# Kernel tuning notes

Measured on AMD Instinct MI355X. Metric: run time of the kernel, lower is better.

Reference implementation:

```python
import jax, jax.numpy as jnp
import numpy as np

B, N = 64, 4096          # trees per batch, leaves per complete binary tree
V, S = 21, 50            # amino-acid vocab, grammar-symbol vocab
E, H = 64, 128           # embed_dim, hidden_dim


def setup_inputs() -> dict:
    key = jax.random.key(0)
    ks = jax.random.split(key, 16)

    def lin_w(k, din, dout):
        return (jax.random.normal(k, (dout, din), jnp.float32) / np.sqrt(din)).astype(jnp.float32)

    tokens = jax.random.randint(ks[0], (B, N), 0, V, dtype=jnp.int32)
    symbols = jax.random.randint(ks[1], (B, N - 1), 0, S, dtype=jnp.int32)

    emb = jax.random.normal(ks[2], (V, E), jnp.float32) * 0.02
    emb = emb.at[0].set(0.0)  # padding_idx=0
    sym_emb = jax.random.normal(ks[3], (S, E), jnp.float32) * 0.02

    return {
        "tokens": tokens, "symbols": symbols,
        "emb": emb, "sym_emb": sym_emb,
        "Wp": lin_w(ks[4], E, H), "bp": jnp.zeros((H,), jnp.float32),
        "Wi": lin_w(ks[5], H, H), "bi": jnp.zeros((H,), jnp.float32),
        "Ui": lin_w(ks[6], H, H),
        "Wf": lin_w(ks[7], H, H), "bf": jnp.zeros((H,), jnp.float32),
        "Uf": lin_w(ks[8], H, H),
        "Wo": lin_w(ks[9], H, H), "bo": jnp.zeros((H,), jnp.float32),
        "Uo": lin_w(ks[10], H, H),
        "Wu": lin_w(ks[11], H, H), "bu": jnp.zeros((H,), jnp.float32),
        "Uu": lin_w(ks[12], H, H),
        "Wout": lin_w(ks[13], H, H), "bout": jnp.zeros((H,), jnp.float32),
    }


def _encode(tokens, symbols, emb, sym_emb, Wp, bp, Wi, bi, Ui, Wf, bf, Uf,
            Wo, bo, Uo, Wu, bu, Uu, Wout, bout):
    emb = emb.at[0].set(0.0)  # padding row contributes nothing (and gets no grad)

    # Leaf nodes: amino-acid embedding -> input_proj, no children.
    x = emb[tokens] @ Wp.T + bp                      # [B, N, H]
    i = jax.nn.sigmoid(x @ Wi.T + bi)
    o = jax.nn.sigmoid(x @ Wo.T + bo)
    u = jnp.tanh(x @ Wu.T + bu)
    c = i * u                                        # [B, N, H]
    h = o * jnp.tanh(c)

    # Bottom-up over levels of the complete binary tree (Child-Sum Tree-LSTM).
    off, n = 0, N
    while n > 1:
        m = n // 2
        xs = sym_emb[symbols[:, off:off + m]] @ Wp.T + bp   # [B, m, H]
        hl, hr = h[:, 0::2], h[:, 1::2]
        cl, cr = c[:, 0::2], c[:, 1::2]
        ht = hl + hr                                         # h_tilde = sum_j h_j
        gi = jax.nn.sigmoid(xs @ Wi.T + bi + ht @ Ui.T)
        go = jax.nn.sigmoid(xs @ Wo.T + bo + ht @ Uo.T)
        gu = jnp.tanh(xs @ Wu.T + bu + ht @ Uu.T)
        fx = xs @ Wf.T + bf
        fl = jax.nn.sigmoid(fx + hl @ Uf.T)                  # per-child forget gates
        fr = jax.nn.sigmoid(fx + hr @ Uf.T)
        c = gi * gu + fl * cl + fr * cr
        h = go * jnp.tanh(c)
        off += m
        n = m

    root_h = h[:, 0]                                         # [B, H]
    return root_h @ Wout.T + bout                            # output_proj


def reference(tokens, symbols, emb, sym_emb, Wp, bp, Wi, bi, Ui, Wf, bf, Uf,
              Wo, bo, Uo, Wu, bu, Uu, Wout, bout):
    return _encode(tokens, symbols, emb, sym_emb, Wp, bp, Wi, bi, Ui, Wf, bf,
                   Uf, Wo, bo, Uo, Wu, bu, Uu, Wout, bout)
```

## Files before the change

### kernel.cpp

```cpp
#include <hip/hip_runtime.h>
#include <hip/hip_bf16.h>

typedef __attribute__((ext_vector_type(8))) short short8;
typedef __attribute__((ext_vector_type(4))) float f32x4;

static constexpr int B_ = 64;
static constexpr int N_ = 4096;
static constexpr int V_ = 21;
static constexpr int S_ = 50;
static constexpr int E_ = 64;
static constexpr int H_ = 128;
static constexpr int NPAIR = V_ * V_;
static constexpr int NTAB = NPAIR * S_;

__device__ __forceinline__ float rcp_(float x) { return __builtin_amdgcn_rcpf(x); }
__device__ __forceinline__ float sigm(float x) { return rcp_(1.0f + __expf(-x)); }
__device__ __forceinline__ float tanh_(float x) {
  float a = fabsf(x);
  float e = __expf(-2.0f * a);
  float t = (1.0f - e) * rcp_(1.0f + e);
  return x < 0.0f ? -t : t;
}
__device__ __forceinline__ unsigned short f2bf(float f) {
  __hip_bfloat16 b = __float2bfloat16(f);
  return *reinterpret_cast<unsigned short*>(&b);
}
__device__ __forceinline__ float bf2f(unsigned short u) {
  return __uint_as_float(((unsigned int)u) << 16);
}

struct Gates { float cv, hv; };
__device__ __forceinline__ Gates gate_combine(float4 sx,
    float i_p, float o_p, float u_p, float fl_p, float fr_p, float cl, float cr) {
  float gi = sigm(sx.x + i_p);
  float go = sigm(sx.y + o_p);
  float gu = tanh_(sx.z + u_p);
  float fl = sigm(sx.w + fl_p);
  float fr = sigm(sx.w + fr_p);
  float cv = fmaf(gi, gu, fmaf(fl, cl, fr * cr));
  Gates g; g.cv = cv; g.hv = go * tanh_(cv);
  return g;
}

__global__ void k_pre0(const float* __restrict__ Ui, const float* __restrict__ Uo,
                       const float* __restrict__ Uu, const float* __restrict__ Uf,
                       const float* __restrict__ Wi, const float* __restrict__ Wo,
                       const float* __restrict__ Wu, const float* __restrict__ Wf,
                       const float* __restrict__ Wp, const float* __restrict__ Wout,
                       unsigned short* __restrict__ Wfrag, float* __restrict__ Wt,
                       float* __restrict__ Wxt, float* __restrict__ Wpt,
                       float* __restrict__ Woutt) {
  int blk = blockIdx.x, t = threadIdx.x;
  if (blk < 32) {
    int idx = blk * 256 + t;
    int L = idx & 63;
    int K = (idx >> 6) & 3;
    int T = idx >> 8;
    int n = 16 * T + (L & 15);
    int k0 = 32 * K + ((L >> 4) << 3);
    int g = n >> 7, o = n & 127;
    const float* U = (g == 0) ? Ui : (g == 1) ? Uo : (g == 2) ? Uu : Uf;
    unsigned short out[8];
    #pragma unroll
    for (int j = 0; j < 8; ++j) out[j] = f2bf(U[o * 128 + k0 + j]);
    *(int4*)(Wfrag + (size_t)idx * 8) = *(int4*)out;
  } else if (blk < 96) {
    bool isU = blk < 64;
    int base = (((blk & 31)) * 256 + t) * 8;
    int k = base >> 9;
    int col = base & 511;
    int gg = col >> 7, o0 = col & 127;
    const float* M;
    if (isU) M = (gg == 0) ? Ui : (gg == 1) ? Uo : (gg == 2) ? Uu : Uf;
    else     M = (gg == 0) ? Wi : (gg == 1) ? Wo : (gg == 2) ? Wu : Wf;
    float* D = isU ? Wt : Wxt;
    float v[8];
    #pragma unroll
    for (int j = 0; j < 8; ++j) v[j] = M[(o0 + j) * 128 + k];
    *(float4*)(D + base) = *(float4*)v;
    *(float4*)(D + base + 4) = *(float4*)(v + 4);
  } else if (blk == 96) {
    for (int i = t; i < E_ * H_; i += 256) {
      int e = i >> 7, o = i & 127;
      Wpt[i] = Wp[o * E_ + e];
    }
  } else {
    for (int i = t; i < H_ * H_; i += 256) {
      int k = i >> 7, o = i & 127;
      Woutt[i] = Wout[o * H_ + k];
    }
  }
}

__global__ void k_pre1(const float* __restrict__ emb, const float* __restrict__ sym_emb,
                       const float* __restrict__ Wpt, const float* __restrict__ Wxt,
                       const float* __restrict__ bp, const float* __restrict__ bi,
                       const float* __restrict__ bo, const float* __restrict__ bu,
                       const float* __restrict__ bfv,
                       unsigned short* __restrict__ leaf_h8, float* __restrict__ leaf_c,
                       float* __restrict__ symx) {
  int blk = blockIdx.x, t = threadIdx.x;
  __shared__ float x[128];
  if (blk < V_) {
    int v = blk;
    float acc = bp[t];
    if (v != 0) {
      for (int e = 0; e < E_; ++e) acc = fmaf(emb[v * E_ + e], Wpt[e * 128 + t], acc);
    }
    x[t] = acc;
    __syncthreads();
    float zi = bi[t], zo = bo[t], zu = bu[t];
    for (int k = 0; k < H_; ++k) {
      float xv = x[k];
      const float* wr = Wxt + k * 512;
      zi = fmaf(xv, wr[t], zi);
      zo = fmaf(xv, wr[128 + t], zo);
      zu = fmaf(xv, wr[256 + t], zu);
    }
    float gi = sigm(zi), go = sigm(zo), gu = tanh_(zu);
    float c = gi * gu;
    leaf_c[v * H_ + t] = c;
    leaf_h8[v * H_ + t] = f2bf(go * tanh_(c));
  } else {
    int s = blk - V_;
    float acc = bp[t];
    for (int e = 0; e < E_; ++e) acc = fmaf(sym_emb[s * E_ + e], Wpt[e * 128 + t], acc);
    x[t] = acc;
    __syncthreads();
    float zi = bi[t], zo = bo[t], zu = bu[t], zf = bfv[t];
    for (int k = 0; k < H_; ++k) {
      float xv = x[k];
      const float* wr = Wxt + k * 512;
      zi = fmaf(xv, wr[t], zi);
      zo = fmaf(xv, wr[128 + t], zo);
      zu = fmaf(xv, wr[256 + t], zu);
      zf = fmaf(xv, wr[384 + t], zf);
    }
    float4 v4 = make_float4(zi, zo, zu, zf);
    *(float4*)(symx + (size_t)s * 512 + t * 4) = v4;
  }
}

__global__ void k_tabA(const unsigned short* __restrict__ leaf_h8, const float* __restrict__ Wt,
                       float* __restrict__ za) {
  int p = blockIdx.x, t = threadIdx.x;
  int tl = p / V_, tr = p % V_;
  __shared__ float hl[128], hr[128];
  hl[t] = bf2f(leaf_h8[tl * H_ + t]);
  hr[t] = bf2f(leaf_h8[tr * H_ + t]);
  __syncthreads();
  float zi = 0.f, zo = 0.f, zu = 0.f, pfl = 0.f, pfr = 0.f;
  for (int k = 0; k < H_; ++k) {
    float l = hl[k], r = hr[k], ht = l + r;
    const float* wr = Wt + k * 512;
    zi = fmaf(ht, wr[t], zi);
    zo = fmaf(ht, wr[128 + t], zo);
    zu = fmaf(ht, wr[256 + t], zu);
    float wf = wr[384 + t];
    pfl = fmaf(l, wf, pfl);
    pfr = fmaf(r, wf, pfr);
  }
  float* z = za + (size_t)p * 640;
  z[t] = zi; z[128 + t] = zo; z[256 + t] = zu; z[384 + t] = pfl; z[512 + t] = pfr;
}

__global__ void k_tabB(const float* __restrict__ za, const float* __restrict__ symx,
                       const float* __restrict__ leaf_c,
                       const int* __restrict__ tokens, const int* __restrict__ symbols,
                       unsigned short* __restrict__ tab_h8, float* __restrict__ tab_c,
                       int* __restrict__ idx1) {
  int blk = blockIdx.x, t = threadIdx.x;
  if (blk < NTAB / 2) {
    int row = blk * 2 + (t >> 7);
    int u = t & 127;
    int p = row / S_, s = row - p * S_;
    int tl = p / V_, tr = p - tl * V_;
    const float* z = za + (size_t)p * 640;
    float4 sx = *(const float4*)(symx + (size_t)s * 512 + u * 4);
    Gates gt = gate_combine(sx, z[u], z[128 + u], z[256 + u], z[384 + u], z[512 + u],
                            leaf_c[tl * H_ + u], leaf_c[tr * H_ + u]);
    tab_c[(size_t)row * H_ + u] = gt.cv;
    tab_h8[(size_t)row * H_ + u] = f2bf(gt.hv);
  } else {
    int g = (blk - NTAB / 2) * 256 + t;
    int b = g >> 11, j = g & 2047;
    idx1[g] = (tokens[b * N_ + 2 * j] * V_ + tokens[b * N_ + 2 * j + 1]) * S_ + symbols[b * (N_ - 1) + j];
  }
}

__global__ void __launch_bounds__(512, 4) k_lvl23(
    const unsigned short* __restrict__ Wfrag, const float* __restrict__ symx,
    const int* __restrict__ symbols, const int* __restrict__ idx1,
    const unsigned short* __restrict__ gh8, const float* __restrict__ gc,
    unsigned short* __restrict__ h_out8, float* __restrict__ c_out) {
  __shared__ __align__(16) unsigned short Ag[64][136];
  __shared__ __align__(16) unsigned short Bh[32][136];
  __shared__ float Bc[32][132];
  int t = threadIdx.x;
  int w = t >> 6, L = t & 63, q = L >> 4, cL = L & 15;
  int cc = 16 * w + cL;
  int g0 = blockIdx.x * 32;
  int b = g0 >> 10;
  int j2 = g0 & 1023;
  const int* sym_b = symbols + (size_t)b * (N_ - 1);
  const int* gix = idx1 + 2 * g0;

  #pragma unroll
  for (int i = 0; i < 2; ++i) {
    int fid = t + 512 * i;
    int row = fid >> 4, co = (fid & 15) * 8;
    *(int4*)&Ag[row][co] = *(const int4*)(gh8 + (size_t)gix[row] * H_ + co);
  }
  __syncthreads();

  const short8* wf = (const short8*)Wfrag;
  #pragma unroll
  for (int c = 0; c < 2; ++c) {
    float clp[4], crp[4];
    int spre[4];
    #pragma unroll
    for (int it = 0; it < 4; ++it) {
      int n = 16 * c + 8 * (it >> 1) + 2 * q + (it & 1);
      clp[it] = gc[(size_t)gix[2 * n] * H_ + cc];
      crp[it] = gc[(size_t)gix[2 * n + 1] * H_ + cc];
      spre[it] = sym_b[2048 + j2 + n];
    }
    f32x4 acc[2][4];
    #pragma unroll
    for (int r = 0; r < 2; ++r)
      #pragma unroll
      for (int g = 0; g < 4; ++g) acc[r][g] = (f32x4){0.f, 0.f, 0.f, 0.f};
    #pragma unroll
    for (int K = 0; K < 4; ++K) {
      short8 bfr[4];
      #pragma unroll
      for (int g = 0; g < 4; ++g) bfr[g] = wf[(size_t)((w + 8 * g) * 4 + K) * 64 + L];
      short8 a0 = *(const short8*)&Ag[32 * c + cL][K * 32 + q * 8];
      short8 a1 = *(const short8*)&Ag[32 * c + 16 + cL][K * 32 + q * 8];
      #pragma unroll
      for (int g = 0; g < 4; ++g) {
        acc[0][g] = __builtin_amdgcn_mfma_f32_16x16x32_bf16(a0, bfr[g], acc[0][g], 0, 0, 0);
        acc[1][g] = __builtin_amdgcn_mfma_f32_16x16x32_bf16(a1, bfr[g], acc[1][g], 0, 0, 0);
      }
    }
    #pragma unroll
    for (int r = 0; r < 2; ++r) {
      #pragma unroll
      for (int nd = 0; nd < 2; ++nd) {
        int it = r * 2 + nd;
        int n = 16 * c + 8 * r + 2 * q + nd;
        float4 sx = *(const float4*)(symx + (size_t)spre[it] * 512 + cc * 4);
        Gates gt = gate_combine(sx,
            acc[r][0][2 * nd] + acc[r][0][2 * nd + 1],
            acc[r][1][2 * nd] + acc[r][1][2 * nd + 1],
            acc[r][2][2 * nd] + acc[r][2][2 * nd + 1],
            acc[r][3][2 * nd], acc[r][3][2 * nd + 1], clp[it], crp[it]);
        Bc[n][cc] = gt.cv;
        Bh[n][cc] = f2bf(gt.hv);
      }
    }
  }
  __syncthreads();
  {
    int spre[4];
    #pragma unroll
    for (int it = 0; it < 4; ++it) {
      int n = 8 * (it >> 1) + 2 * q + (it & 1);
      spre[it] = sym_b[3072 + (j2 >> 1) + n];
    }
    f32x4 acc[2][4];
    #pragma unroll
    for (int r = 0; r < 2; ++r)
      #pragma unroll
      for (int g = 0; g < 4; ++g) acc[r][g] = (f32x4){0.f, 0.f, 0.f, 0.f};
    #pragma unroll
    for (int K = 0; K < 4; ++K) {
      short8 bfr[4];
      #pragma unroll
      for (int g = 0; g < 4; ++g) bfr[g] = wf[(size_t)((w + 8 * g) * 4 + K) * 64 + L];
      short8 a0 = *(const short8*)&Bh[cL][K * 32 + q * 8];
      short8 a1 = *(const short8*)&Bh[16 + cL][K * 32 + q * 8];
      #pragma unroll
      for (int g = 0; g < 4; ++g) {
        acc[0][g] = __builtin_amdgcn_mfma_f32_16x16x32_bf16(a0, bfr[g], acc[0][g], 0, 0, 0);
        acc[1][g] = __builtin_amdgcn_mfma_f32_16x16x32_bf16(a1, bfr[g], acc[1][g], 0, 0, 0);
      }
    }
    #pragma unroll
    for (int r = 0; r < 2; ++r) {
      #pragma unroll
      for (int nd = 0; nd < 2; ++nd) {
        int it = r * 2 + nd;
        int n = 8 * r + 2 * q + nd;
        int G3 = (g0 >> 1) + n;
        float4 sx = *(const float4*)(symx + (size_t)spre[it] * 512 + cc * 4);
        Gates gt = gate_combine(sx,
            acc[r][0][2 * nd] + acc[r][0][2 * nd + 1],
            acc[r][1][2 * nd] + acc[r][1][2 * nd + 1],
            acc[r][2][2 * nd] + acc[r][2][2 * nd + 1],
            acc[r][3][2 * nd], acc[r][3][2 * nd + 1],
            Bc[2 * n][cc], Bc[2 * n + 1][cc]);
        c_out[(size_t)G3 * H_ + cc] = gt.cv;
        h_out8[(size_t)G3 * H_ + cc] = f2bf(gt.hv);
      }
    }
  }
}

__global__ void __launch_bounds__(512, 2) k_mid(
    const unsigned short* __restrict__ Wfrag, const float* __restrict__ symx,
    const int* __restrict__ symbols,
    const unsigned short* __restrict__ in_h8, const float* __restrict__ in_c,
    unsigned short* __restrict__ out_h8, float* __restrict__ out_c) {
  __shared__ __align__(16) unsigned short Ah0[64][136];
  __shared__ __align__(16) unsigned short Ah1[32][136];
  __shared__ float Cs0[64][128];
  __shared__ float Cs1[32][128];
  int t = threadIdx.x;
  int w = t >> 6, L = t & 63, q = L >> 4, cL = L & 15;
  int cc = 16 * w + cL;
  int blk = blockIdx.x;
  int b = blk >> 3, sub = blk & 7;
  size_t base3 = (size_t)blk * 64;

  #pragma unroll
  for (int i = 0; i < 2; ++i) {
    int fid = t + 512 * i;
    int row = fid >> 4, co = (fid & 15) * 8;
    *(int4*)&Ah0[row][co] = *(const int4*)(in_h8 + (base3 + row) * H_ + co);
  }
  #pragma unroll
  for (int i = 0; i < 4; ++i) {
    int fid = t + 512 * i;
    int row = fid >> 5, c4 = (fid & 31) << 2;
    *(float4*)&Cs0[row][c4] = *(const float4*)(in_c + (base3 + row) * H_ + c4);
  }
  __syncthreads();

  const short8* wf = (const short8*)Wfrag;
  int R = 64;
  #pragma unroll
  for (int lev = 0; lev < 6; ++lev) {
    const int l = 4 + lev;
    const int nodes = R >> 1;
    const int jb = b * (N_ - 1) + (N_ - (N_ >> (l - 1))) + ((sub * 32) >> lev);
    unsigned short (*Ard)[136] = (lev & 1) ? Ah1 : Ah0;
    unsigned short (*Awr)[136] = (lev & 1) ? Ah0 : Ah1;
    const float* crd = (lev & 1) ? &Cs1[0][0] : &Cs0[0][0];
    float* cwr = (lev & 1) ? &Cs0[0][0] : &Cs1[0][0];
    const int nchunk = (nodes + 15) >> 4;
    for (int c = 0; c < nchunk; ++c) {
      int spre[4];
      #pragma unroll
      for (int it = 0; it < 4; ++it) {
        int n = 16 * c + 8 * (it >> 1) + 2 * q + (it & 1);
        spre[it] = (n < nodes) ? symbols[jb + n] : 0;
      }
      f32x4 acc[2][4];
      #pragma unroll
      for (int r = 0; r < 2; ++r)
        #pragma unroll
        for (int g = 0; g < 4; ++g) acc[r][g] = (f32x4){0.f, 0.f, 0.f, 0.f};
      const bool useA1 = (2 * nodes - 32 * c) > 16;
      #pragma unroll
      for (int K = 0; K < 4; ++K) {
        short8 bfr[4];
        #pragma unroll
        for (int g = 0; g < 4; ++g) bfr[g] = wf[(size_t)((w + 8 * g) * 4 + K) * 64 + L];
        short8 a0 = *(const short8*)&Ard[32 * c + cL][K * 32 + q * 8];
        #pragma unroll
        for (int g = 0; g < 4; ++g)
          acc[0][g] = __builtin_amdgcn_mfma_f32_16x16x32_bf16(a0, bfr[g], acc[0][g], 0, 0, 0);
        if (useA1) {
          short8 a1 = *(const short8*)&Ard[32 * c + 16 + cL][K * 32 + q * 8];
          #pragma unroll
          for (int g = 0; g < 4; ++g)
            acc[1][g] = __builtin_amdgcn_mfma_f32_16x16x32_bf16(a1, bfr[g], acc[1][g], 0, 0, 0);
        }
      }
      #pragma unroll
      for (int r = 0; r < 2; ++r) {
        #pragma unroll
        for (int nd = 0; nd < 2; ++nd) {
          int it = r * 2 + nd;
          int n = 16 * c + 8 * r + 2 * q + nd;
          if (n < nodes) {
            float4 sx = *(const float4*)(symx + (size_t)spre[it] * 512 + cc * 4);
            Gates gt = gate_combine(sx,
                acc[r][0][2 * nd] + acc[r][0][2 * nd + 1],
                acc[r][1][2 * nd] + acc[r][1][2 * nd + 1],
                acc[r][2][2 * nd] + acc[r][2][2 * nd + 1],
                acc[r][3][2 * nd], acc[r][3][2 * nd + 1],
                crd[(size_t)(2 * n) * 128 + cc], crd[(size_t)(2 * n + 1) * 128 + cc]);
            if (lev == 5) {
              out_c[(size_t)blk * H_ + cc] = gt.cv;
              out_h8[(size_t)blk * H_ + cc] = f2bf(gt.hv);
            } else {
              cwr[(size_t)n * 128 + cc] = gt.cv;
              Awr[n][cc] = f2bf(gt.hv);
            }
          }
        }
      }
    }
    __syncthreads();
    R >>= 1;
  }
}

__global__ void __launch_bounds__(512, 2) k_fin(
    const unsigned short* __restrict__ Wfrag, const float* __restrict__ symx,
    const int* __restrict__ symbols,
    const unsigned short* __restrict__ in_h8, const float* __restrict__ in_c,
    const float* __restrict__ Woutt, const float* __restrict__ bout,
    float* __restrict__ out) {
  __shared__ __align__(16) unsigned short Ah0[8][136];
  __shared__ __align__(16) unsigned short Ah1[4][136];
  __shared__ float Cs0[8][128];
  __shared__ float Cs1[4][128];
  __shared__ float rootv[128];
  int t = threadIdx.x;
  int w = t >> 6, L = t & 63, q = L >> 4, cL = L & 15;
  int cc = 16 * w + cL;
  int b = blockIdx.x;

  if (t < 128) {
    int row = t >> 4, co = (t & 15) * 8;
    *(int4*)&Ah0[row][co] = *(const int4*)(in_h8 + (size_t)(b * 8 + row) * H_ + co);
  }
  if (t < 256) {
    int row = t >> 5, c4 = (t & 31) << 2;
    *(float4*)&Cs0[row][c4] = *(const float4*)(in_c + (size_t)(b * 8 + row) * H_ + c4);
  }
  __syncthreads();

  const short8* wf = (const short8*)Wfrag;
  int R = 8;
  #pragma unroll
  for (int lev = 0; lev < 3; ++lev) {
    const int l = 10 + lev;
    const int nodes = R >> 1;
    const int jb = b * (N_ - 1) + (N_ - (N_ >> (l - 1)));
    unsigned short (*Ard)[136] = (lev & 1) ? Ah1 : Ah0;
    unsigned short (*Awr)[136] = (lev & 1) ? Ah0 : Ah1;
    const float* crd = (lev & 1) ? &Cs1[0][0] : &Cs0[0][0];
    float* cwr = (lev & 1) ? &Cs0[0][0] : &Cs1[0][0];
    int spre[4];
    #pragma unroll
    for (int it = 0; it < 4; ++it) {
      int n = 8 * (it >> 1) + 2 * q + (it & 1);
      spre[it] = (n < nodes) ? symbols[jb + n] : 0;
    }
    f32x4 acc[4];
    #pragma unroll
    for (int g = 0; g < 4; ++g) acc[g] = (f32x4){0.f, 0.f, 0.f, 0.f};
    #pragma unroll
    for (int K = 0; K < 4; ++K) {
      short8 bfr[4];
      #pragma unroll
      for (int g = 0; g < 4; ++g) bfr[g] = wf[(size_t)((w + 8 * g) * 4 + K) * 64 + L];
      short8 a0 = *(const short8*)&Ard[cL & 7][K * 32 + q * 8];
      #pragma unroll
      for (int g = 0; g < 4; ++g)
        acc[g] = __builtin_amdgcn_mfma_f32_16x16x32_bf16(a0, bfr[g], acc[g], 0, 0, 0);
    }
    #pragma unroll
    for (int nd = 0; nd < 2; ++nd) {
      int it = nd;
      int n = 2 * q + nd;
      if (n < nodes) {
        float4 sx = *(const float4*)(symx + (size_t)spre[it] * 512 + cc * 4);
        Gates gt = gate_combine(sx,
            acc[0][2 * nd] + acc[0][2 * nd + 1],
            acc[1][2 * nd] + acc[1][2 * nd + 1],
            acc[2][2 * nd] + acc[2][2 * nd + 1],
            acc[3][2 * nd], acc[3][2 * nd + 1],
            crd[(size_t)(2 * n) * 128 + cc], crd[(size_t)(2 * n + 1) * 128 + cc]);
        if (lev == 2) {
          rootv[cc] = gt.hv;
        } else {
          cwr[(size_t)n * 128 + cc] = gt.cv;
          Awr[n][cc] = f2bf(gt.hv);
        }
      }
    }
    __syncthreads();
    R >>= 1;
  }
  if (t < 128) {
    float acc = bout[t];
    for (int k = 0; k < H_; ++k) acc = fmaf(rootv[k], Woutt[k * 128 + t], acc);
    out[(size_t)b * H_ + t] = acc;
  }
}

extern "C" void kernel_launch(void* const* d_in, const int* in_sizes, int n_in,
                              void* d_out, int out_size, void* d_ws, size_t ws_size,
                              hipStream_t stream) {
  const int* tokens    = (const int*)d_in[0];
  const int* symbols   = (const int*)d_in[1];
  const float* emb     = (const float*)d_in[2];
  const float* sym_emb = (const float*)d_in[3];
  const float* Wp  = (const float*)d_in[4];
  const float* bp  = (const float*)d_in[5];
  const float* Wi  = (const float*)d_in[6];
  const float* bi  = (const float*)d_in[7];
  const float* Ui  = (const float*)d_in[8];
  const float* Wf  = (const float*)d_in[9];
  const float* bf  = (const float*)d_in[10];
  const float* Uf  = (const float*)d_in[11];
  const float* Wo  = (const float*)d_in[12];
  const float* bo  = (const float*)d_in[13];
  const float* Uo  = (const float*)d_in[14];
  const float* Wu  = (const float*)d_in[15];
  const float* bu  = (const float*)d_in[16];
  const float* Uu  = (const float*)d_in[17];
  const float* Wout= (const float*)d_in[18];
  const float* bout= (const float*)d_in[19];

  char* ws = (char*)d_ws;
  unsigned short* Wfrag   = (unsigned short*)(ws);
  float*          Wt      = (float*)(ws + 131072);
  float*          Wxt     = (float*)(ws + 393216);
  float*          Wpt     = (float*)(ws + 655360);
  float*          Woutt   = (float*)(ws + 688128);
  unsigned short* leaf_h8 = (unsigned short*)(ws + 753664);
  float*          leaf_c  = (float*)(ws + 759040);
  float*          symx    = (float*)(ws + 769792);
  float*          za      = (float*)(ws + 872192);
  unsigned short* tab_h8  = (unsigned short*)(ws + 2001152UL);
  float*          tab_c   = (float*)(ws + 7645952UL);
  int*            idx1    = (int*)(ws + 18935552UL);
  unsigned short* L3h8    = (unsigned short*)(ws + 19459840UL);
  float*          L3c     = (float*)(ws + 27848448UL);
  unsigned short* L9h8    = (unsigned short*)(ws + 44625664UL);
  float*          L9c     = (float*)(ws + 44756736UL);

  k_pre0<<<98, 256, 0, stream>>>(Ui, Uo, Uu, Uf, Wi, Wo, Wu, Wf, Wp, Wout,
                                 Wfrag, Wt, Wxt, Wpt, Woutt);
  k_pre1<<<V_ + S_, 128, 0, stream>>>(emb, sym_emb, Wpt, Wxt,
                                      bp, bi, bo, bu, bf, leaf_h8, leaf_c, symx);
  k_tabA<<<NPAIR, 128, 0, stream>>>(leaf_h8, Wt, za);
  k_tabB<<<NTAB / 2 + 512, 256, 0, stream>>>(za, symx, leaf_c, tokens, symbols,
                                             tab_h8, tab_c, idx1);
  k_lvl23<<<2048, 512, 0, stream>>>(Wfrag, symx, symbols, idx1, tab_h8, tab_c, L3h8, L3c);
  k_mid<<<512, 512, 0, stream>>>(Wfrag, symx, symbols, L3h8, L3c, L9h8, L9c);
  k_fin<<<B_, 512, 0, stream>>>(Wfrag, symx, symbols, L9h8, L9c, Woutt, bout,
                                (float*)d_out);
}
```

Baseline: 221.7 us.

## Exploit linearity to precompute per-leaf U projections, dropping pair-table kernel

The per-pair matmul kernel (441 pairs × 128-dim products) is replaced by per-leaf projections P_leaf = h_leaf·U^T computed inside k_pre1, since U(hl+hr) = U hl + U hr. tabB then sums two per-leaf rows instead of reading a precomputed pair row. The weight-transpose kernel now stages tiles through shared memory for coalesced writes, and the pre-kernels use 512-thread blocks. This removes one kernel launch and most of the redundant pair arithmetic, at the cost of extra adds and a few more loads in tabB.

```diff
diff --git a/kernel.cpp b/kernel.cpp
--- a/kernel.cpp
+++ b/kernel.cpp
@@ -42,17 +42,19 @@
   return g;
 }
 
-__global__ void k_pre0(const float* __restrict__ Ui, const float* __restrict__ Uo,
-                       const float* __restrict__ Uu, const float* __restrict__ Uf,
-                       const float* __restrict__ Wi, const float* __restrict__ Wo,
-                       const float* __restrict__ Wu, const float* __restrict__ Wf,
-                       const float* __restrict__ Wp, const float* __restrict__ Wout,
-                       unsigned short* __restrict__ Wfrag, float* __restrict__ Wt,
-                       float* __restrict__ Wxt, float* __restrict__ Wpt,
-                       float* __restrict__ Woutt) {
+__global__ void __launch_bounds__(512) k_pre0(
+    const float* __restrict__ Ui, const float* __restrict__ Uo,
+    const float* __restrict__ Uu, const float* __restrict__ Uf,
+    const float* __restrict__ Wi, const float* __restrict__ Wo,
+    const float* __restrict__ Wu, const float* __restrict__ Wf,
+    const float* __restrict__ Wp, const float* __restrict__ Wout,
+    unsigned short* __restrict__ Wfrag, float* __restrict__ Wt,
+    float* __restrict__ Wxt, float* __restrict__ Wpt,
+    float* __restrict__ Woutt) {
+  __shared__ float Tt[32][129];
   int blk = blockIdx.x, t = threadIdx.x;
-  if (blk < 32) {
-    int idx = blk * 256 + t;
+  if (blk < 16) {
+    int idx = blk * 512 + t;
     int L = idx & 63;
     int K = (idx >> 6) & 3;
     int T = idx >> 8;
@@ -64,107 +66,110 @@
     #pragma unroll
     for (int j = 0; j < 8; ++j) out[j] = f2bf(U[o * 128 + k0 + j]);
     *(int4*)(Wfrag + (size_t)idx * 8) = *(int4*)out;
-  } else if (blk < 96) {
-    bool isU = blk < 64;
-    int base = (((blk & 31)) * 256 + t) * 8;
-    int k = base >> 9;
-    int col = base & 511;
-    int gg = col >> 7, o0 = col & 127;
-    const float* M;
-    if (isU) M = (gg == 0) ? Ui : (gg == 1) ? Uo : (gg == 2) ? Uu : Uf;
-    else     M = (gg == 0) ? Wi : (gg == 1) ? Wo : (gg == 2) ? Wu : Wf;
-    float* D = isU ? Wt : Wxt;
-    float v[8];
-    #pragma unroll
-    for (int j = 0; j < 8; ++j) v[j] = M[(o0 + j) * 128 + k];
-    *(float4*)(D + base) = *(float4*)v;
-    *(float4*)(D + base + 4) = *(float4*)(v + 4);
-  } else if (blk == 96) {
-    for (int i = t; i < E_ * H_; i += 256) {
+  } else if (blk < 48) {
+    int job = blk - 16;
+    int m = job >> 2, kt = job & 3;
+    int k0 = kt * 32;
+    const float* M = (m == 0) ? Ui : (m == 1) ? Uo : (m == 2) ? Uu : (m == 3) ? Uf
+                   : (m == 4) ? Wi : (m == 5) ? Wo : (m == 6) ? Wu : Wf;
+    float* D = (m < 4) ? Wt : Wxt;
+    int g = m & 3;
+    #pragma unroll
+    for (int pass = 0; pass < 2; ++pass) {
+      int o = (t >> 3) + 64 * pass;
+      int kk = 4 * (t & 7);
+      float4 v = *(const float4*)(M + o * 128 + k0 + kk);
+      Tt[kk][o] = v.x; Tt[kk + 1][o] = v.y; Tt[kk + 2][o] = v.z; Tt[kk + 3][o] = v.w;
+    }
+    __syncthreads();
+    #pragma unroll
+    for (int pass = 0; pass < 8; ++pass) {
+      int kk = pass * 4 + (t >> 7);
+      int o = t & 127;
+      D[(size_t)(k0 + kk) * 512 + g * 128 + o] = Tt[kk][o];
+    }
+  } else if (blk == 48) {
+    for (int i = t; i < E_ * H_; i += 512) {
       int e = i >> 7, o = i & 127;
       Wpt[i] = Wp[o * E_ + e];
     }
   } else {
-    for (int i = t; i < H_ * H_; i += 256) {
+    for (int i = t; i < H_ * H_; i += 512) {
       int k = i >> 7, o = i & 127;
       Woutt[i] = Wout[o * H_ + k];
     }
   }
 }
 
-__global__ void k_pre1(const float* __restrict__ emb, const float* __restrict__ sym_emb,
-                       const float* __restrict__ Wpt, const float* __restrict__ Wxt,
-                       const float* __restrict__ bp, const float* __restrict__ bi,
-                       const float* __restrict__ bo, const float* __restrict__ bu,
-                       const float* __restrict__ bfv,
-                       unsigned short* __restrict__ leaf_h8, float* __restrict__ leaf_c,
-                       float* __restrict__ symx) {
+__global__ void __launch_bounds__(512) k_pre1(
+    const float* __restrict__ emb, const float* __restrict__ sym_emb,
+    const float* __restrict__ Wpt, const float* __restrict__ Wxt,
+    const float* __restrict__ Wt,
+    const float* __restrict__ bp, const float* __restrict__ bi,
+    const float* __restrict__ bo, const float* __restrict__ bu,
+    const float* __restrict__ bfv,
+    unsigned short* __restrict__ leaf_h8, float* __restrict__ leaf_c,
+    float* __restrict__ symx, float* __restrict__ P_leaf) {
+  __shared__ float x[128];
+  __shared__ float zs[512];
+  __shared__ float hl[128];
   int blk = blockIdx.x, t = threadIdx.x;
-  __shared__ float x[128];
   if (blk < V_) {
     int v = blk;
-    float acc = bp[t];
-    if (v != 0) {
-      for (int e = 0; e < E_; ++e) acc = fmaf(emb[v * E_ + e], Wpt[e * 128 + t], acc);
-    }
-    x[t] = acc;
-    __syncthreads();
-    float zi = bi[t], zo = bo[t], zu = bu[t];
-    for (int k = 0; k < H_; ++k) {
-      float xv = x[k];
-      const float* wr = Wxt + k * 512;
-      zi = fmaf(xv, wr[t], zi);
-      zo = fmaf(xv, wr[128 + t], zo);
-      zu = fmaf(xv, wr[256 + t], zu);
-    }
-    float gi = sigm(zi), go = sigm(zo), gu = tanh_(zu);
-    float c = gi * gu;
-    leaf_c[v * H_ + t] = c;
-    leaf_h8[v * H_ + t] = f2bf(go * tanh_(c));
+    if (t < 128) {
+      float acc = bp[t];
+      if (v != 0) {
+        for (int e = 0; e < E_; ++e) acc = fmaf(emb[v * E_ + e], Wpt[e * 128 + t], acc);
+      }
+      x[t] = acc;
+    }
+    __syncthreads();
+    if (t < 384) {
+      int g = t >> 7;
+      const float* bb = (g == 0) ? bi : (g == 1) ? bo : bu;
+      float z = bb[t & 127];
+      for (int k = 0; k < H_; ++k) z = fmaf(x[k], Wxt[k * 512 + t], z);
+      zs[t] = z;
+    }
+    __syncthreads();
+    if (t < 128) {
+      float gi = sigm(zs[t]), go = sigm(zs[128 + t]), gu = tanh_(zs[256 + t]);
+      float c = gi * gu;
+      leaf_c[v * H_ + t] = c;
+      unsigned short hb = f2bf(go * tanh_(c));
+      leaf_h8[v * H_ + t] = hb;
+      hl[t] = bf2f(hb);
+    }
+    __syncthreads();
+    {
+      float z = 0.f;
+      for (int k = 0; k < H_; ++k) z = fmaf(hl[k], Wt[k * 512 + t], z);
+      P_leaf[(size_t)v * 512 + t] = z;
+    }
   } else {
     int s = blk - V_;
-    float acc = bp[t];
-    for (int e = 0; e < E_; ++e) acc = fmaf(sym_emb[s * E_ + e], Wpt[e * 128 + t], acc);
-    x[t] = acc;
-    __syncthreads();
-    float zi = bi[t], zo = bo[t], zu = bu[t], zf = bfv[t];
-    for (int k = 0; k < H_; ++k) {
-      float xv = x[k];
-      const float* wr = Wxt + k * 512;
-      zi = fmaf(xv, wr[t], zi);
-      zo = fmaf(xv, wr[128 + t], zo);
-      zu = fmaf(xv, wr[256 + t], zu);
-      zf = fmaf(xv, wr[384 + t], zf);
-    }
-    float4 v4 = make_float4(zi, zo, zu, zf);
-    *(float4*)(symx + (size_t)s * 512 + t * 4) = v4;
-  }
-}
-
-__global__ void k_tabA(const unsigned short* __restrict__ leaf_h8, const float* __restrict__ Wt,
-                       float* __restrict__ za) {
-  int p = blockIdx.x, t = threadIdx.x;
-  int tl = p / V_, tr = p % V_;
-  __shared__ float hl[128], hr[128];
-  hl[t] = bf2f(leaf_h8[tl * H_ + t]);
-  hr[t] = bf2f(leaf_h8[tr * H_ + t]);
-  __syncthreads();
-  float zi = 0.f, zo = 0.f, zu = 0.f, pfl = 0.f, pfr = 0.f;
-  for (int k = 0; k < H_; ++k) {
-    float l = hl[k], r = hr[k], ht = l + r;
-    const float* wr = Wt + k * 512;
-    zi = fmaf(ht, wr[t], zi);
-    zo = fmaf(ht, wr[128 + t], zo);
-    zu = fmaf(ht, wr[256 + t], zu);
-    float wf = wr[384 + t];
-    pfl = fmaf(l, wf, pfl);
-    pfr = fmaf(r, wf, pfr);
-  }
-  float* z = za + (size_t)p * 640;
-  z[t] = zi; z[128 + t] = zo; z[256 + t] = zu; z[384 + t] = pfl; z[512 + t] = pfr;
-}
-
-__global__ void k_tabB(const float* __restrict__ za, const float* __restrict__ symx,
+    if (t < 128) {
+      float acc = bp[t];
+      for (int e = 0; e < E_; ++e) acc = fmaf(sym_emb[s * E_ + e], Wpt[e * 128 + t], acc);
+      x[t] = acc;
+    }
+    __syncthreads();
+    {
+      int g = t >> 7;
+      const float* bb = (g == 0) ? bi : (g == 1) ? bo : (g == 2) ? bu : bfv;
+      float z = bb[t & 127];
+      for (int k = 0; k < H_; ++k) z = fmaf(x[k], Wxt[k * 512 + t], z);
+      zs[t] = z;
+    }
+    __syncthreads();
+    if (t < 128) {
+      float4 v4 = make_float4(zs[t], zs[128 + t], zs[256 + t], zs[384 + t]);
+      *(float4*)(symx + (size_t)s * 512 + t * 4) = v4;
+    }
+  }
+}
+
+__global__ void k_tabB(const float* __restrict__ P_leaf, const float* __restrict__ symx,
                        const float* __restrict__ leaf_c,
                        const int* __restrict__ tokens, const int* __restrict__ symbols,
                        unsigned short* __restrict__ tab_h8, float* __restrict__ tab_c,
@@ -175,10 +180,13 @@
     int u = t & 127;
     int p = row / S_, s = row - p * S_;
     int tl = p / V_, tr = p - tl * V_;
-    const float* z = za + (size_t)p * 640;
+    const float* Pl = P_leaf + (size_t)tl * 512;
+    const float* Pr = P_leaf + (size_t)tr * 512;
     float4 sx = *(const float4*)(symx + (size_t)s * 512 + u * 4);
-    Gates gt = gate_combine(sx, z[u], z[128 + u], z[256 + u], z[384 + u], z[512 + u],
-                            leaf_c[tl * H_ + u], leaf_c[tr * H_ + u]);
+    Gates gt = gate_combine(sx,
+        Pl[u] + Pr[u], Pl[128 + u] + Pr[128 + u], Pl[256 + u] + Pr[256 + u],
+        Pl[384 + u], Pr[384 + u],
+        leaf_c[tl * H_ + u], leaf_c[tr * H_ + u]);
     tab_c[(size_t)row * H_ + u] = gt.cv;
     tab_h8[(size_t)row * H_ + u] = f2bf(gt.hv);
   } else {
@@ -527,7 +535,7 @@
   unsigned short* leaf_h8 = (unsigned short*)(ws + 753664);
   float*          leaf_c  = (float*)(ws + 759040);
   float*          symx    = (float*)(ws + 769792);
-  float*          za      = (float*)(ws + 872192);
+  float*          P_leaf  = (float*)(ws + 872192);
   unsigned short* tab_h8  = (unsigned short*)(ws + 2001152UL);
   float*          tab_c   = (float*)(ws + 7645952UL);
   int*            idx1    = (int*)(ws + 18935552UL);
@@ -536,12 +544,12 @@
   unsigned short* L9h8    = (unsigned short*)(ws + 44625664UL);
   float*          L9c     = (float*)(ws + 44756736UL);
 
-  k_pre0<<<98, 256, 0, stream>>>(Ui, Uo, Uu, Uf, Wi, Wo, Wu, Wf, Wp, Wout,
+  k_pre0<<<50, 512, 0, stream>>>(Ui, Uo, Uu, Uf, Wi, Wo, Wu, Wf, Wp, Wout,
                                  Wfrag, Wt, Wxt, Wpt, Woutt);
-  k_pre1<<<V_ + S_, 128, 0, stream>>>(emb, sym_emb, Wpt, Wxt,
-                                      bp, bi, bo, bu, bf, leaf_h8, leaf_c, symx);
-  k_tabA<<<NPAIR, 128, 0, stream>>>(leaf_h8, Wt, za);
-  k_tabB<<<NTAB / 2 + 512, 256, 0, stream>>>(za, symx, leaf_c, tokens, symbols,
+  k_pre1<<<V_ + S_, 512, 0, stream>>>(emb, sym_emb, Wpt, Wxt, Wt,
+                                      bp, bi, bo, bu, bf,
+                                      leaf_h8, leaf_c, symx, P_leaf);
+  k_tabB<<<NTAB / 2 + 512, 256, 0, stream>>>(P_leaf, symx, leaf_c, tokens, symbols,
                                              tab_h8, tab_c, idx1);
   k_lvl23<<<2048, 512, 0, stream>>>(Wfrag, symx, symbols, idx1, tab_h8, tab_c, L3h8, L3c);
   k_mid<<<512, 512, 0, stream>>>(Wfrag, symx, symbols, L3h8, L3c, L9h8, L9c);
```

Measured after the change: 216.2 us. 2.5% less time.
